# Kernel tuning notes

Hardware: AMD Instinct MI355X
Metric: run time of the kernel (lower is better)

## Reference

```python
import jax, jax.numpy as jnp
import numpy as np

HIDDEN = 1024
HEADS = 16
HEAD_DIM = HIDDEN // HEADS


def setup_inputs() -> dict:
    key = jax.random.key(0)
    ks = jax.random.split(key, 9)
    B, S, D = 8, 1370, HIDDEN
    x = jax.random.normal(ks[0], (B, S, D), dtype=jnp.float32)
    s = 1.0 / np.sqrt(D)
    Wq = jax.random.normal(ks[1], (D, D), dtype=jnp.float32) * s
    bq = jnp.zeros((D,), dtype=jnp.float32)
    Wk = jax.random.normal(ks[2], (D, D), dtype=jnp.float32) * s
    bk = jnp.zeros((D,), dtype=jnp.float32)
    Wv = jax.random.normal(ks[3], (D, D), dtype=jnp.float32) * s
    bv = jnp.zeros((D,), dtype=jnp.float32)
    Wo = jax.random.normal(ks[4], (D, D), dtype=jnp.float32) * s
    bo = jnp.zeros((D,), dtype=jnp.float32)
    return {"x": x, "Wq": Wq, "bq": bq, "Wk": Wk, "bk": bk,
            "Wv": Wv, "bv": bv, "Wo": Wo, "bo": bo}


def reference(x, Wq, bq, Wk, bk, Wv, bv, Wo, bo):
    B, S, D = x.shape
    H, Dh = HEADS, HEAD_DIM
    # separate Q/K/V projections
    q = (x @ Wq + bq).reshape(B, S, H, Dh).transpose(0, 2, 1, 3)  # [B,H,S,Dh]
    k = (x @ Wk + bk).reshape(B, S, H, Dh).transpose(0, 2, 1, 3)
    v = (x @ Wv + bv).reshape(B, S, H, Dh).transpose(0, 2, 1, 3)
    scale = jnp.asarray(Dh, q.dtype) ** -0.5
    attn = jnp.einsum('bhqd,bhkd->bhqk', q, k) * scale  # [B,H,S,S]
    attn = jax.nn.softmax(attn, axis=-1)
    out = jnp.einsum('bhqk,bhkd->bhqd', attn, v)        # [B,H,S,Dh]
    out = out.transpose(0, 2, 1, 3).reshape(B, S, D)
    return out @ Wo + bo
```

## Files before the change

### kernel.cpp

```cpp
#include <hip/hip_runtime.h>
#include <stdint.h>

#define DEV __device__ __forceinline__

typedef unsigned short u16;
typedef __attribute__((ext_vector_type(8))) __bf16 bf16x8;
typedef __attribute__((ext_vector_type(8))) u16 u16x8;
typedef __attribute__((ext_vector_type(4))) u16 u16x4;
typedef __attribute__((ext_vector_type(4))) float floatx4;

#define S_LEN 1370
#define S_PAD 1408
#define NH 16
#define DH 64
#define M_TOK (8 * S_LEN)
#define NKT (S_PAD / 64)
#define CEXP 0.18033688f

DEV u16 f2bf(float f) {
    union { float f; uint32_t u; } v; v.f = f;
    uint32_t u = v.u + 0x7fffu + ((v.u >> 16) & 1u);
    return (u16)(u >> 16);
}

typedef const __attribute__((address_space(1))) void as1_cvoid;
typedef __attribute__((address_space(3))) void as3_void;

DEV void async16(const void* g, void* s) {
    __builtin_amdgcn_global_load_lds((as1_cvoid*)g, (as3_void*)s, 16, 0, 0);
}

__global__ void cvt_bf16(const float* __restrict__ src, u16* __restrict__ dst) {
    const size_t i0 = ((size_t)blockIdx.x * 256 + threadIdx.x) * 8;
    const float4 a = *(const float4*)(src + i0);
    const float4 b = *(const float4*)(src + i0 + 4);
    u16x8 o;
    o[0] = f2bf(a.x); o[1] = f2bf(a.y); o[2] = f2bf(a.z); o[3] = f2bf(a.w);
    o[4] = f2bf(b.x); o[5] = f2bf(b.y); o[6] = f2bf(b.z); o[7] = f2bf(b.w);
    *(u16x8*)(dst + i0) = o;
}

__global__ void transpose4(const float* __restrict__ w0, const float* __restrict__ w1,
                           const float* __restrict__ w2, const float* __restrict__ w3,
                           u16* __restrict__ t0, u16* __restrict__ t1,
                           u16* __restrict__ t2, u16* __restrict__ t3) {
    __shared__ u16 tile[64][65];
    const float* src; u16* dst;
    switch (blockIdx.z) {
        case 0: src = w0; dst = t0; break;
        case 1: src = w1; dst = t1; break;
        case 2: src = w2; dst = t2; break;
        default: src = w3; dst = t3; break;
    }
    const int tx = blockIdx.x, ty = blockIdx.y, tid = threadIdx.x;
#pragma unroll
    for (int i = 0; i < 16; i++) {
        int e = i * 256 + tid, r = e >> 6, c = e & 63;
        tile[r][c] = f2bf(src[(size_t)(ty * 64 + r) * 1024 + tx * 64 + c]);
    }
    __syncthreads();
#pragma unroll
    for (int i = 0; i < 16; i++) {
        int e = i * 256 + tid, r = e >> 6, c = e & 63;
        dst[(size_t)(tx * 64 + r) * 1024 + ty * 64 + c] = tile[c][r];
    }
}

#define GEMM_KLOOP(M_, N_)                                                     \
    floatx4 acc[4][4];                                                         \
    _Pragma("unroll")                                                          \
    for (int i = 0; i < 4; i++)                                                \
        _Pragma("unroll")                                                      \
        for (int j = 0; j < 4; j++) acc[i][j] = (floatx4){0.f, 0.f, 0.f, 0.f}; \
    const int srow = tid >> 2;                                                 \
    const int kb = ((tid & 3) ^ ((tid >> 3) & 3)) * 16;     \
    const int rsw = (quad ^ ((l15 >> 1) & 3)) * 8;          \
    int ar0 = mbase + srow;          if (ar0 > (M_) - 1) ar0 = (M_) - 1;       \
    int ar1 = mbase + 64 + srow;     if (ar1 > (M_) - 1) ar1 = (M_) - 1;       \
    int br0 = nbase + srow;          if (br0 > (N_) - 1) br0 = (N_) - 1;       \
    int br1 = nbase + 64 + srow;     if (br1 > (N_) - 1) br1 = (N_) - 1;       \
    const char* pA = (const char*)A;                                           \
    const char* pB = (const char*)BT;                                          \
    char* ldsA = (char*)As + w * 1024;                                         \
    char* ldsB = (char*)Bs + w * 1024;                                         \
    for (int kt = 0; kt < 32; kt++) {                                          \
        const int koff = kt * 64 + kb;                                         \
        async16(pA + (size_t)ar0 * 2048 + koff, ldsA);                         \
        async16(pA + (size_t)ar1 * 2048 + koff, ldsA + 4096);                  \
        async16(pB + (size_t)br0 * 2048 + koff, ldsB);                         \
        async16(pB + (size_t)br1 * 2048 + koff, ldsB + 4096);                  \
        __syncthreads();                                                       \
        bf16x8 af[4], bfv[4];                                                  \
        _Pragma("unroll")                                                      \
        for (int mi = 0; mi < 4; mi++)                                         \
            af[mi] = __builtin_bit_cast(bf16x8,                                \
                *(const u16x8*)&As[(wm + mi * 16 + l15) * 32 + rsw]);          \
        _Pragma("unroll")                                                      \
        for (int ni = 0; ni < 4; ni++)                                         \
            bfv[ni] = __builtin_bit_cast(bf16x8,                               \
                *(const u16x8*)&Bs[(wn + ni * 16 + l15) * 32 + rsw]);          \
        _Pragma("unroll")                                                      \
        for (int mi = 0; mi < 4; mi++)                                         \
            _Pragma("unroll")                                                  \
            for (int ni = 0; ni < 4; ni++)                                     \
                acc[mi][ni] = __builtin_amdgcn_mfma_f32_16x16x32_bf16(         \
                    af[mi], bfv[ni], acc[mi][ni], 0, 0, 0);                    \
        __syncthreads();                                                       \
    }

__global__ void gemm_qkv(const u16* __restrict__ A, const u16* __restrict__ BT,
                         const float* __restrict__ bq, const float* __restrict__ bk,
                         const float* __restrict__ bv, u16* __restrict__ Cq,
                         u16* __restrict__ Ck, u16* __restrict__ VT, int M) {
    __shared__ u16 As[128 * 32];
    __shared__ u16 Bs[128 * 32];
    const int tid = threadIdx.x;
    const int w = tid >> 6, lane = tid & 63, quad = lane >> 4, l15 = lane & 15;
    const int mbase = blockIdx.x * 128, nbase = blockIdx.y * 128;
    const int wm = (w >> 1) * 64, wn = (w & 1) * 64;

    GEMM_KLOOP(M, 3072)

    const int sel = nbase >> 10;
    if (sel == 0) {
#pragma unroll
        for (int ni = 0; ni < 4; ni++) {
            const int n = nbase + wn + ni * 16 + l15;
            const float bb = bq[n];
#pragma unroll
            for (int mi = 0; mi < 4; mi++)
#pragma unroll
                for (int r = 0; r < 4; r++) {
                    const int m = mbase + wm + mi * 16 + quad * 4 + r;
                    if (m < M) Cq[(size_t)m * 1024 + n] = f2bf((acc[mi][ni][r] + bb) * CEXP);
                }
        }
    } else if (sel == 1) {
#pragma unroll
        for (int ni = 0; ni < 4; ni++) {
            const int n = nbase - 1024 + wn + ni * 16 + l15;
            const float bb = bk[n];
#pragma unroll
            for (int mi = 0; mi < 4; mi++)
#pragma unroll
                for (int r = 0; r < 4; r++) {
                    const int m = mbase + wm + mi * 16 + quad * 4 + r;
                    if (m < M) Ck[(size_t)m * 1024 + n] = f2bf(acc[mi][ni][r] + bb);
                }
        }
    } else {
#pragma unroll
        for (int ni = 0; ni < 4; ni++) {
            const int fe = nbase - 2048 + wn + ni * 16 + l15;
            const float bb = bv[fe];
            const int hh = fe >> 6, dd = fe & 63;
#pragma unroll
            for (int mi = 0; mi < 4; mi++)
#pragma unroll
                for (int r = 0; r < 4; r++) {
                    const int m = mbase + wm + mi * 16 + quad * 4 + r;
                    if (m < M) {
                        const int btk = m / S_LEN;
                        const int ss = m - btk * S_LEN;
                        VT[(size_t)((btk * NH + hh) * DH + dd) * S_PAD + ss] =
                            f2bf(acc[mi][ni][r] + bb);
                    }
                }
        }
    }
}

__global__ void gemm_o(const u16* __restrict__ A, const u16* __restrict__ BT,
                       const float* __restrict__ bias, float* __restrict__ C, int M) {
    __shared__ u16 As[128 * 32];
    __shared__ u16 Bs[128 * 32];
    const int tid = threadIdx.x;
    const int w = tid >> 6, lane = tid & 63, quad = lane >> 4, l15 = lane & 15;
    const int mbase = blockIdx.x * 128, nbase = blockIdx.y * 128;
    const int wm = (w >> 1) * 64, wn = (w & 1) * 64;

    GEMM_KLOOP(M, 1024)

#pragma unroll
    for (int ni = 0; ni < 4; ni++) {
        const int n = nbase + wn + ni * 16 + l15;
        const float bb = bias[n];
#pragma unroll
        for (int mi = 0; mi < 4; mi++)
#pragma unroll
            for (int r = 0; r < 4; r++) {
                const int m = mbase + wm + mi * 16 + quad * 4 + r;
                if (m < M) C[(size_t)m * 1024 + n] = acc[mi][ni][r] + bb;
            }
    }
}

__global__ void flash_attn(const u16* __restrict__ Q, const u16* __restrict__ K,
                           const u16* __restrict__ VT, u16* __restrict__ O) {
    __shared__ u16 Ks[2][2 * 64 * 32];
    __shared__ u16 Vs[2][2 * 64 * 32];
    __shared__ u16 Ps[4][32 * 72];

    const int tid = threadIdx.x;
    const int w = tid >> 6, lane = tid & 63, quad = lane >> 4, l15 = lane & 15;
    const int bh = blockIdx.x, b = bh >> 4, h = bh & 15;
    const int q0 = blockIdx.y * 128 + w * 32;

    bf16x8 qf[2][2];
#pragma unroll
    for (int mi = 0; mi < 2; mi++) {
        int qr = q0 + mi * 16 + l15;
        if (qr > S_LEN - 1) qr = S_LEN - 1;
        const u16* qp = Q + (size_t)(b * S_LEN + qr) * 1024 + h * 64 + quad * 8;
        qf[mi][0] = __builtin_bit_cast(bf16x8, *(const u16x8*)qp);
        qf[mi][1] = __builtin_bit_cast(bf16x8, *(const u16x8*)(qp + 32));
    }

    floatx4 o_acc[2][4];
#pragma unroll
    for (int mi = 0; mi < 2; mi++)
#pragma unroll
        for (int nd = 0; nd < 4; nd++) o_acc[mi][nd] = (floatx4){0.f, 0.f, 0.f, 0.f};
    float lacc[2] = {0.f, 0.f};

    const int lrow = lane >> 2;
    const int scol = ((lane & 3) ^ ((lane >> 3) & 3)) * 16;
    const char* Kbl = (const char*)K + ((size_t)b * S_LEN * 1024 + h * 64) * 2 + scol;
    const char* Vbl = (const char*)VT +
                      ((size_t)(bh * 64 + w * 16 + lrow) * S_PAD) * 2 + scol;
    char* KsB = (char*)Ks;
    char* VsB = (char*)Vs;
    u16* Pw = Ps[w];

    const int rcol = (quad ^ ((l15 >> 1) & 3)) * 16;

#define STAGE(KT, BI)                                                          \
    {                                                                          \
        int key_ = (KT) * 64 + w * 16 + lrow;                                  \
        if (key_ > S_LEN - 1) key_ = S_LEN - 1;                                \
        const char* kg_ = Kbl + (size_t)key_ * 2048;                           \
        char* kd_ = KsB + (BI) * 8192 + (w * 16) * 64;                         \
        async16(kg_, kd_);                                                     \
        async16(kg_ + 64, kd_ + 4096);                                         \
        const char* vg_ = Vbl + (KT) * 128;                                    \
        char* vd_ = VsB + (BI) * 8192 + (w * 16) * 64;                         \
        async16(vg_, vd_);                                                     \
        async16(vg_ + 64, vd_ + 4096);                                         \
    }

    STAGE(0, 0)
    __syncthreads();

    for (int kt = 0; kt < NKT; kt++) {
        const int bi = kt & 1;
        if (kt + 1 < NKT) STAGE(kt + 1, bi ^ 1)
        const char* KsT = KsB + bi * 8192;
        const char* VsT = VsB + bi * 8192;

        floatx4 st[2][4];
#pragma unroll
        for (int mi = 0; mi < 2; mi++)
#pragma unroll
            for (int ni = 0; ni < 4; ni++) st[mi][ni] = (floatx4){0.f, 0.f, 0.f, 0.f};
#pragma unroll
        for (int kk = 0; kk < 2; kk++)
#pragma unroll
            for (int ni = 0; ni < 4; ni++) {
                bf16x8 kf = __builtin_bit_cast(bf16x8,
                    *(const u16x8*)(KsT + kk * 4096 + (ni * 16 + l15) * 64 + rcol));
                st[0][ni] = __builtin_amdgcn_mfma_f32_16x16x32_bf16(kf, qf[0][kk], st[0][ni], 0, 0, 0);
                st[1][ni] = __builtin_amdgcn_mfma_f32_16x16x32_bf16(kf, qf[1][kk], st[1][ni], 0, 0, 0);
            }

        if (kt == NKT - 1) {
#pragma unroll
            for (int ni = 0; ni < 4; ni++)
#pragma unroll
                for (int r = 0; r < 4; r++) {
                    const bool oob = (kt * 64 + ni * 16 + quad * 4 + r) >= S_LEN;
                    if (oob) { st[0][ni][r] = -16384.f; st[1][ni][r] = -16384.f; }
                }
        }

#pragma unroll
        for (int mi = 0; mi < 2; mi++)
#pragma unroll
            for (int ni = 0; ni < 4; ni++) {
                u16x4 pq;
#pragma unroll
                for (int r = 0; r < 4; r++) {
                    const float p = __builtin_amdgcn_exp2f(st[mi][ni][r]);
                    lacc[mi] += p;
                    union { float f; uint32_t u; } cv; cv.f = p;
                    pq[r] = (u16)((cv.u + 0x8000u) >> 16);
                }
                *(u16x4*)&Pw[(mi * 16 + l15) * 72 + ni * 16 + quad * 4] = pq;
            }

        __asm__ __volatile__("" ::: "memory");

#pragma unroll
        for (int kk = 0; kk < 2; kk++) {
            bf16x8 pf0 = __builtin_bit_cast(bf16x8,
                *(const u16x8*)&Pw[(l15) * 72 + kk * 32 + quad * 8]);
            bf16x8 pf1 = __builtin_bit_cast(bf16x8,
                *(const u16x8*)&Pw[(16 + l15) * 72 + kk * 32 + quad * 8]);
#pragma unroll
            for (int nd = 0; nd < 4; nd++) {
                bf16x8 vf = __builtin_bit_cast(bf16x8,
                    *(const u16x8*)(VsT + kk * 4096 + (nd * 16 + l15) * 64 + rcol));
                o_acc[0][nd] = __builtin_amdgcn_mfma_f32_16x16x32_bf16(pf0, vf, o_acc[0][nd], 0, 0, 0);
                o_acc[1][nd] = __builtin_amdgcn_mfma_f32_16x16x32_bf16(pf1, vf, o_acc[1][nd], 0, 0, 0);
            }
        }
        __syncthreads();
    }

    float linv[2];
#pragma unroll
    for (int mi = 0; mi < 2; mi++) {
        float rs = lacc[mi];
        rs += __shfl_xor(rs, 16);
        rs += __shfl_xor(rs, 32);
        linv[mi] = 1.f / rs;
    }

#pragma unroll
    for (int mi = 0; mi < 2; mi++)
#pragma unroll
        for (int r = 0; r < 4; r++) {
            const float inv = __shfl(linv[mi], quad * 4 + r);
            const int q = q0 + mi * 16 + quad * 4 + r;
            if (q < S_LEN) {
                u16* op = O + (size_t)(b * S_LEN + q) * 1024 + h * 64;
#pragma unroll
                for (int nd = 0; nd < 4; nd++)
                    op[nd * 16 + l15] = f2bf(o_acc[mi][nd][r] * inv);
            }
        }
}

extern "C" void kernel_launch(void* const* d_in, const int* in_sizes, int n_in,
                              void* d_out, int out_size, void* d_ws, size_t ws_size,
                              hipStream_t stream) {
    const float* x  = (const float*)d_in[0];
    const float* Wq = (const float*)d_in[1];
    const float* bq = (const float*)d_in[2];
    const float* Wk = (const float*)d_in[3];
    const float* bk = (const float*)d_in[4];
    const float* Wv = (const float*)d_in[5];
    const float* bv = (const float*)d_in[6];
    const float* Wo = (const float*)d_in[7];
    const float* bo = (const float*)d_in[8];
    float* out = (float*)d_out;

    u16* WqT = (u16*)d_ws;
    u16* WkT = WqT + (size_t)1024 * 1024;
    u16* WvT = WkT + (size_t)1024 * 1024;
    u16* WoT = WvT + (size_t)1024 * 1024;
    u16* xb  = WoT + (size_t)1024 * 1024;
    u16* Qb  = xb + (size_t)M_TOK * 1024;
    u16* Kb  = Qb + (size_t)M_TOK * 1024;
    u16* VTb = Kb + (size_t)M_TOK * 1024;
    u16* Ob  = VTb + (size_t)128 * 64 * S_PAD;

    cvt_bf16<<<dim3(M_TOK * 1024 / 2048), 256, 0, stream>>>(x, xb);
    transpose4<<<dim3(16, 16, 4), 256, 0, stream>>>(Wq, Wk, Wv, Wo, WqT, WkT, WvT, WoT);
    gemm_qkv<<<dim3(86, 24), 256, 0, stream>>>(xb, WqT, bq, bk, bv, Qb, Kb, VTb, M_TOK);
    flash_attn<<<dim3(128, 11), 256, 0, stream>>>(Qb, Kb, VTb, Ob);
    gemm_o<<<dim3(86, 8), 256, 0, stream>>>(Ob, WoT, bo, out, M_TOK);
}
```

Measured before the change: 378.9 us.

## Double-buffer LDS tiles in projection GEMM k-loop to overlap loads with MFMA

The shared-memory A/B tiles in the QKV and output-projection GEMMs now have two buffers. The next k-tile is issued asynchronously while MFMAs run on the current one, and one barrier per iteration is dropped. This is meant to hide global-load latency behind compute, at the cost of doubling LDS use per block, which may reduce occupancy. The async copies of the next tile may not be waited on before the barrier, so correctness depends on how async16 is implemented.

```diff
diff --git a/kernel.cpp b/kernel.cpp
--- a/kernel.cpp
+++ b/kernel.cpp
@@ -83,22 +83,33 @@
     const char* pB = (const char*)BT;                                          \
     char* ldsA = (char*)As + w * 1024;                                         \
     char* ldsB = (char*)Bs + w * 1024;                                         \
+    {                                                                          \
+        async16(pA + (size_t)ar0 * 2048 + kb, ldsA);                           \
+        async16(pA + (size_t)ar1 * 2048 + kb, ldsA + 4096);                    \
+        async16(pB + (size_t)br0 * 2048 + kb, ldsB);                           \
+        async16(pB + (size_t)br1 * 2048 + kb, ldsB + 4096);                    \
+    }                                                                          \
+    __syncthreads();                                                           \
     for (int kt = 0; kt < 32; kt++) {                                          \
-        const int koff = kt * 64 + kb;                                         \
-        async16(pA + (size_t)ar0 * 2048 + koff, ldsA);                         \
-        async16(pA + (size_t)ar1 * 2048 + koff, ldsA + 4096);                  \
-        async16(pB + (size_t)br0 * 2048 + koff, ldsB);                         \
-        async16(pB + (size_t)br1 * 2048 + koff, ldsB + 4096);                  \
-        __syncthreads();                                                       \
+        const int bi = kt & 1;                                                 \
+        if (kt + 1 < 32) {                                                     \
+            const int koff = (kt + 1) * 64 + kb;                               \
+            const int bo = (bi ^ 1) * 8192;                                    \
+            async16(pA + (size_t)ar0 * 2048 + koff, ldsA + bo);                \
+            async16(pA + (size_t)ar1 * 2048 + koff, ldsA + bo + 4096);         \
+            async16(pB + (size_t)br0 * 2048 + koff, ldsB + bo);                \
+            async16(pB + (size_t)br1 * 2048 + koff, ldsB + bo + 4096);         \
+        }                                                                      \
+        const int bu = bi * 4096;                                              \
         bf16x8 af[4], bfv[4];                                                  \
         _Pragma("unroll")                                                      \
         for (int mi = 0; mi < 4; mi++)                                         \
             af[mi] = __builtin_bit_cast(bf16x8,                                \
-                *(const u16x8*)&As[(wm + mi * 16 + l15) * 32 + rsw]);          \
+                *(const u16x8*)&As[bu + (wm + mi * 16 + l15) * 32 + rsw]);     \
         _Pragma("unroll")                                                      \
         for (int ni = 0; ni < 4; ni++)                                         \
             bfv[ni] = __builtin_bit_cast(bf16x8,                               \
-                *(const u16x8*)&Bs[(wn + ni * 16 + l15) * 32 + rsw]);          \
+                *(const u16x8*)&Bs[bu + (wn + ni * 16 + l15) * 32 + rsw]);     \
         _Pragma("unroll")                                                      \
         for (int mi = 0; mi < 4; mi++)                                         \
             _Pragma("unroll")                                                  \
@@ -112,8 +123,8 @@
                          const float* __restrict__ bq, const float* __restrict__ bk,
                          const float* __restrict__ bv, u16* __restrict__ Cq,
                          u16* __restrict__ Ck, u16* __restrict__ VT, int M) {
-    __shared__ u16 As[128 * 32];
-    __shared__ u16 Bs[128 * 32];
+    __shared__ u16 As[2 * 128 * 32];
+    __shared__ u16 Bs[2 * 128 * 32];
     const int tid = threadIdx.x;
     const int w = tid >> 6, lane = tid & 63, quad = lane >> 4, l15 = lane & 15;
     const int mbase = blockIdx.x * 128, nbase = blockIdx.y * 128;
@@ -172,8 +183,8 @@
 
 __global__ void gemm_o(const u16* __restrict__ A, const u16* __restrict__ BT,
                        const float* __restrict__ bias, float* __restrict__ C, int M) {
-    __shared__ u16 As[128 * 32];
-    __shared__ u16 Bs[128 * 32];
+    __shared__ u16 As[2 * 128 * 32];
+    __shared__ u16 Bs[2 * 128 * 32];
     const int tid = threadIdx.x;
     const int w = tid >> 6, lane = tid & 63, quad = lane >> 4, l15 = lane & 15;
     const int mbase = blockIdx.x * 128, nbase = blockIdx.y * 128;
```

Measured after the change: 381.2 us. Within noise of the previous version (+0.6%).
